# Kernel optimization log

Hardware: AMD Instinct MI355X
Metric: run time of the kernel (lower is better)

The kernel has to match this reference:

```python
import jax, jax.numpy as jnp
import numpy as np

B, V, F_IN, F_HID, F_OUT = 16384, 64, 5, 3, 1

def setup_inputs() -> dict:
    key = jax.random.key(0)
    kA, kh, kw1, kw2 = jax.random.split(key, 4)
    A = jax.random.uniform(kA, (B, V, V), dtype=jnp.float32)
    h0 = jax.random.normal(kh, (B, V, F_IN), dtype=jnp.float32)
    sd1 = np.sqrt(1.0 / (F_IN + F_HID))
    sd2 = np.sqrt(1.0 / (F_HID + F_OUT))
    W1 = jax.random.uniform(kw1, (F_IN, F_HID), dtype=jnp.float32, minval=-sd1, maxval=sd1)
    W2 = jax.random.uniform(kw2, (F_HID, F_OUT), dtype=jnp.float32, minval=-sd2, maxval=sd2)
    return {"A": A, "h0": h0, "W1": W1, "W2": W2}

def reference(A, h0, W1, W2):
    # adj_hat = A + I
    eye = jnp.eye(A.shape[-1], dtype=A.dtype)
    adj_hat = A + eye
    # D^{-1/2} of rowsums of adj_hat; A_nrm = D^{-1/2} adj_hat D^{-1/2}
    dinv = jnp.sum(adj_hat, axis=-1) ** -0.5            # [B, V]
    A_nrm = dinv[:, :, None] * adj_hat * dinv[:, None, :]
    # GCN layer 1: relu(A_nrm @ (h0 @ W1))
    H_first = jax.nn.relu(jnp.einsum('bvw,bwf->bvf', A_nrm, h0 @ W1))  # [B, V, 3]
    # sum pooling over nodes -> [B, 1, 3]
    pooled = jnp.sum(H_first, axis=1, keepdims=True)
    # dense GCN (NN_flag=1, no A matmul, no activation)
    out = pooled @ W2                                    # [B, 1, 1]
    return out
```

## Files before the change

### kernel.cpp

```cpp
#include <hip/hip_runtime.h>
#include <hip/hip_bf16.h>


#define V 64

template<int CTRL>
__device__ __forceinline__ float dpp_row_add(float x) {
    int s = __builtin_amdgcn_update_dpp(0, __float_as_int(x), CTRL, 0xF, 0xF, true);
    return x + __int_as_float(s);
}

__device__ __forceinline__ float reduce16(float x) {
    x = dpp_row_add<0x111>(x);
    x = dpp_row_add<0x112>(x);
    x = dpp_row_add<0x114>(x);
    x = dpp_row_add<0x118>(x);
    return x;
}

__global__ __launch_bounds__(64, 3) void gcn_fused_kernel(
    const float* __restrict__ A,
    const float* __restrict__ h0,
    const float* __restrict__ W1,
    const float* __restrict__ W2,
    float* __restrict__ out)
{
    __shared__ float dinv_lds[V];
    __shared__ float xs_lds[3][V];

    const int b = blockIdx.x;
    const int t = threadIdx.x;
    const int g = t >> 4;
    const int c = t & 15;

    const float* h0b = h0 + (size_t)b * (V * 5) + t * 5;
    float h[5];
    #pragma unroll
    for (int k = 0; k < 5; ++k) h[k] = h0b[k];

    const float4* A4 = reinterpret_cast<const float4*>(A + (size_t)b * (V * V));
    float4 a[16];
    #pragma unroll
    for (int i = 0; i < 16; ++i) a[i] = A4[t + 64 * i];

    float dvr[16];
    #pragma unroll
    for (int i = 0; i < 16; ++i) {
        float p = (a[i].x + a[i].y) + (a[i].z + a[i].w);
        p = reduce16(p);
        float dv = rsqrtf(1.0f + p);
        dvr[i] = dv;
        if (c == 15) dinv_lds[4 * i + g] = dv;
    }

    float dv_t = dinv_lds[t];
    float x0 = 0.f, x1 = 0.f, x2 = 0.f;
    #pragma unroll
    for (int k = 0; k < 5; ++k) {
        float hk = h[k];
        x0 += hk * W1[k * 3 + 0];
        x1 += hk * W1[k * 3 + 1];
        x2 += hk * W1[k * 3 + 2];
    }
    xs_lds[0][t] = dv_t * x0;
    xs_lds[1][t] = dv_t * x1;
    xs_lds[2][t] = dv_t * x2;

    float q0[4], q1[4], q2[4];
    #pragma unroll
    for (int j = 0; j < 4; ++j) {
        q0[j] = xs_lds[0][4 * c + j];
        q1[j] = xs_lds[1][4 * c + j];
        q2[j] = xs_lds[2][4 * c + j];
    }
    float xg0 = (g == 0) ? q0[0] : (g == 1) ? q0[1] : (g == 2) ? q0[2] : q0[3];
    float xg1 = (g == 0) ? q1[0] : (g == 1) ? q1[1] : (g == 2) ? q1[2] : q1[3];
    float xg2 = (g == 0) ? q2[0] : (g == 1) ? q2[1] : (g == 2) ? q2[2] : q2[3];

    const float w20 = W2[0], w21 = W2[1], w22 = W2[2];
    float total = 0.f;
    #pragma unroll
    for (int i = 0; i < 16; ++i) {
        float p0 = a[i].x * q0[0] + a[i].y * q0[1] + a[i].z * q0[2] + a[i].w * q0[3];
        float p1 = a[i].x * q1[0] + a[i].y * q1[1] + a[i].z * q1[2] + a[i].w * q1[3];
        float p2 = a[i].x * q2[0] + a[i].y * q2[1] + a[i].z * q2[2] + a[i].w * q2[3];
        bool diag = (c == i);
        p0 += diag ? xg0 : 0.f;
        p1 += diag ? xg1 : 0.f;
        p2 += diag ? xg2 : 0.f;
        p0 = reduce16(p0);
        p1 = reduce16(p1);
        p2 = reduce16(p2);
        float dv = dvr[i];
        float y = fmaxf(dv * p0, 0.f) * w20
                + fmaxf(dv * p1, 0.f) * w21
                + fmaxf(dv * p2, 0.f) * w22;
        total += (c == 15) ? y : 0.f;
    }

    #pragma unroll
    for (int off = 1; off < 64; off <<= 1) total += __shfl_xor(total, off);
    if (t == 0) out[b] = total;
}

extern "C" void kernel_launch(void* const* d_in, const int* in_sizes, int n_in,
                              void* d_out, int out_size, void* d_ws, size_t ws_size,
                              hipStream_t stream) {
    const float* A  = (const float*)d_in[0];
    const float* h0 = (const float*)d_in[1];
    const float* W1 = (const float*)d_in[2];
    const float* W2 = (const float*)d_in[3];
    float* out = (float*)d_out;

    const int B = in_sizes[0] / (V * V);
    gcn_fused_kernel<<<B, 64, 0, stream>>>(A, h0, W1, W2, out);
}
```

Measured before the change: 50.54 us.

## Pack four graphs per block and trim register and shuffle use

Each block now holds four wavefronts, one per batch graph, with per-wave LDS slices, so fewer blocks are launched and more waves can be resident per CU. The per-row dinv register array is dropped and its values are reread from LDS in the second loop to lower register pressure. The final full-wave shuffle reduction becomes two xor steps, since only lanes with c==15 hold nonzero values. The output write assumes B is divisible by four, and there are no barriers because each wave only touches its own LDS slice.

New measurement: 50.59 us. No clear change (+0.1%).

```diff
diff --git a/kernel.cpp b/kernel.cpp
--- a/kernel.cpp
+++ b/kernel.cpp
@@ -3,6 +3,7 @@
 
 
 #define V 64
+#define WPB 4
 
 template<int CTRL>
 __device__ __forceinline__ float dpp_row_add(float x) {
@@ -18,20 +19,21 @@
     return x;
 }
 
-__global__ __launch_bounds__(64, 3) void gcn_fused_kernel(
+__global__ __launch_bounds__(64 * WPB, 4) void gcn_fused_kernel(
     const float* __restrict__ A,
     const float* __restrict__ h0,
     const float* __restrict__ W1,
     const float* __restrict__ W2,
     float* __restrict__ out)
 {
-    __shared__ float dinv_lds[V];
-    __shared__ float xs_lds[3][V];
+    __shared__ float dinv_lds[WPB][V];
+    __shared__ float xs_lds[WPB][3][V];
 
-    const int b = blockIdx.x;
-    const int t = threadIdx.x;
-    const int g = t >> 4;
-    const int c = t & 15;
+    const int wv = threadIdx.x >> 6;
+    const int t  = threadIdx.x & 63;
+    const int b  = blockIdx.x * WPB + wv;
+    const int g  = t >> 4;
+    const int c  = t & 15;
 
     const float* h0b = h0 + (size_t)b * (V * 5) + t * 5;
     float h[5];
@@ -43,17 +45,14 @@
     #pragma unroll
     for (int i = 0; i < 16; ++i) a[i] = A4[t + 64 * i];
 
-    float dvr[16];
     #pragma unroll
     for (int i = 0; i < 16; ++i) {
         float p = (a[i].x + a[i].y) + (a[i].z + a[i].w);
         p = reduce16(p);
-        float dv = rsqrtf(1.0f + p);
-        dvr[i] = dv;
-        if (c == 15) dinv_lds[4 * i + g] = dv;
+        if (c == 15) dinv_lds[wv][4 * i + g] = rsqrtf(1.0f + p);
     }
 
-    float dv_t = dinv_lds[t];
+    float dv_t = dinv_lds[wv][t];
     float x0 = 0.f, x1 = 0.f, x2 = 0.f;
     #pragma unroll
     for (int k = 0; k < 5; ++k) {
@@ -62,16 +61,16 @@
         x1 += hk * W1[k * 3 + 1];
         x2 += hk * W1[k * 3 + 2];
     }
-    xs_lds[0][t] = dv_t * x0;
-    xs_lds[1][t] = dv_t * x1;
-    xs_lds[2][t] = dv_t * x2;
+    xs_lds[wv][0][t] = dv_t * x0;
+    xs_lds[wv][1][t] = dv_t * x1;
+    xs_lds[wv][2][t] = dv_t * x2;
 
     float q0[4], q1[4], q2[4];
     #pragma unroll
     for (int j = 0; j < 4; ++j) {
-        q0[j] = xs_lds[0][4 * c + j];
-        q1[j] = xs_lds[1][4 * c + j];
-        q2[j] = xs_lds[2][4 * c + j];
+        q0[j] = xs_lds[wv][0][4 * c + j];
+        q1[j] = xs_lds[wv][1][4 * c + j];
+        q2[j] = xs_lds[wv][2][4 * c + j];
     }
     float xg0 = (g == 0) ? q0[0] : (g == 1) ? q0[1] : (g == 2) ? q0[2] : q0[3];
     float xg1 = (g == 0) ? q1[0] : (g == 1) ? q1[1] : (g == 2) ? q1[2] : q1[3];
@@ -91,16 +90,16 @@
         p0 = reduce16(p0);
         p1 = reduce16(p1);
         p2 = reduce16(p2);
-        float dv = dvr[i];
+        float dv = dinv_lds[wv][4 * i + g];
         float y = fmaxf(dv * p0, 0.f) * w20
                 + fmaxf(dv * p1, 0.f) * w21
                 + fmaxf(dv * p2, 0.f) * w22;
         total += (c == 15) ? y : 0.f;
     }
 
-    #pragma unroll
-    for (int off = 1; off < 64; off <<= 1) total += __shfl_xor(total, off);
-    if (t == 0) out[b] = total;
+    total += __shfl_xor(total, 16);
+    total += __shfl_xor(total, 32);
+    if (t == 15) out[b] = total;
 }
 
 extern "C" void kernel_launch(void* const* d_in, const int* in_sizes, int n_in,
@@ -113,5 +112,5 @@
     float* out = (float*)d_out;
 
     const int B = in_sizes[0] / (V * V);
-    gcn_fused_kernel<<<B, 64, 0, stream>>>(A, h0, W1, W2, out);
+    gcn_fused_kernel<<<B / WPB, 64 * WPB, 0, stream>>>(A, h0, W1, W2, out);
 }
```
